# Performance work log

Hardware: AMD Instinct MI355X
Metric: run time of the kernel (lower is better)

Reference implementation:

```python
import jax, jax.numpy as jnp
import numpy as np

DT = 0.005
BETA = 0.9
THR = 0.5
TAU_MIN = 0.02
TAU_STEP = 0.03
TAU_R = 0.002
SLOPE = 25.0  # snntorch fast_sigmoid default surrogate slope

@jax.custom_vjp
def spike_fn(x):
    return (x > 0).astype(x.dtype)

def _spike_fwd(x):
    return spike_fn(x), x

def _spike_bwd(x, g):
    return (g / (SLOPE * jnp.abs(x) + 1.0) ** 2,)

spike_fn.defvjp(_spike_fwd, _spike_bwd)

def setup_inputs() -> dict:
    key = jax.random.key(0)
    ks = jax.random.split(key, 8)
    T, NIN, H, NOUT, P = 1000, 4, 4096, 2, 16
    inv_sqrt_h = 1.0 / np.sqrt(H).astype(np.float32)
    return {
        "x": jax.random.normal(ks[0], (T, NIN + 2, 1), jnp.float32),
        "noise": jax.random.normal(ks[1], (T, H, 1), jnp.float32),
        "Win": jax.random.normal(ks[2], (H, NIN + 2), jnp.float32),
        "Wout": jax.random.normal(ks[3], (NOUT, H), jnp.float32) * inv_sqrt_h,
        "pin": jax.random.normal(ks[4], (H, P), jnp.float32) * inv_sqrt_h,
        "pout": jax.random.normal(ks[5], (H, P), jnp.float32) * inv_sqrt_h,
        "l": jax.random.normal(ks[6], (P,), jnp.float32) * inv_sqrt_h,
        "sigmoid_tau_d": jax.random.normal(ks[7], (H, 1), jnp.float32),
    }

def reference(x, noise, Win, Wout, pin, pout, l, sigmoid_tau_d):
    H = Win.shape[0]
    tau_d = jax.nn.sigmoid(sigmoid_tau_d) * TAU_STEP + TAU_MIN   # [H,1]
    Wr = (l * pin) @ pout.T                                      # [H,H] low-rank recurrent matrix
    decay_r = jnp.exp(jnp.asarray(-DT / TAU_R, x.dtype))         # scalar
    decay_d = jnp.exp(-DT / tau_d)                               # [H,1]
    s_gain = DT / (tau_d * TAU_R)                                # [H,1]

    def step(carry, inp):
        mem, r, s = carry
        xi, ni = inp
        I = Win @ xi + Wr @ r + ni / 10.0                        # [H,1]
        # snntorch Leaky, reset_mechanism='subtract': reset from incoming mem (detached)
        reset = jax.lax.stop_gradient(spike_fn(mem - THR))
        mem = BETA * mem + I - reset * THR
        spk = spike_fn(mem - THR)
        s = s * decay_r + s_gain * spk
        r = decay_d * r + DT * s
        return (mem, r, s), r

    z = jnp.zeros((H, 1), x.dtype)
    _, R = jax.lax.scan(step, (z, z, z), (x, noise))             # R: [T,H,1]
    y = jnp.einsum('oh,thj->toj', Wout, R)                       # [T,O,1]
    return y
```

## Files before the change

kernel.cpp:

```cpp
#include <hip/hip_runtime.h>
#include <math.h>

#define KB       4
#define NBOOT    32
#define NTHREADS 256
#define NW       4
#define HID      4096
#define HB       (HID / KB)
#define NPT      4
#define TT       1000
#define PP       16
#define SLOTW    32

#define BETA 0.9f
#define THRV 0.5f
#define DTV  0.005f

template<int CTRL>
__device__ __forceinline__ float dppx(float v) {
    return __int_as_float(__builtin_amdgcn_update_dpp(
        0, __float_as_int(v), CTRL, 0xF, 0xF, true));
}

__device__ __forceinline__ unsigned long long AL(const unsigned long long* p) {
    return __hip_atomic_load(p, __ATOMIC_RELAXED, __HIP_MEMORY_SCOPE_AGENT);
}
__device__ __forceinline__ void AS(unsigned long long* p, unsigned long long v) {
    __hip_atomic_store(p, v, __ATOMIC_RELAXED, __HIP_MEMORY_SCOPE_AGENT);
}
__device__ __forceinline__ void st64_sc0(unsigned long long* p, unsigned long long v) {
    asm volatile("global_store_dwordx2 %0, %1, off sc0" :: "v"(p), "v"(v) : "memory");
}
__device__ __forceinline__ void rmw3_sc0(unsigned long long* p0,
                                         unsigned long long* p1,
                                         unsigned long long* p2,
                                         unsigned long long& v0,
                                         unsigned long long& v1,
                                         unsigned long long& v2) {
    unsigned long long z = 0;
    asm volatile("global_atomic_add_x2 %0, %3, %6, off sc0\n\t"
                 "global_atomic_add_x2 %1, %4, %6, off sc0\n\t"
                 "global_atomic_add_x2 %2, %5, %6, off sc0\n\t"
                 "s_waitcnt vmcnt(0)"
                 : "=&v"(v0), "=&v"(v1), "=&v"(v2)
                 : "v"(p0), "v"(p1), "v"(p2), "v"(z)
                 : "memory");
}

__global__ void zero_kernel(unsigned* boot) {
    int i = threadIdx.x;
    if (i < NBOOT) boot[i] = 0u;
}

__global__ __launch_bounds__(NTHREADS, 1)
void snn_kernel(const float* __restrict__ x,
                const float* __restrict__ noise,
                const float* __restrict__ Win,
                const float* __restrict__ Wout,
                const float* __restrict__ pin,
                const float* __restrict__ pout,
                const float* __restrict__ lvec,
                const float* __restrict__ stdv,
                float* __restrict__ out,
                unsigned long long* __restrict__ slotsL2,
                unsigned long long* __restrict__ slotsAG,
                unsigned* __restrict__ boot)
{
    const int tid  = threadIdx.x;
    const int wave = tid >> 6;
    const int lane = tid & 63;

    unsigned xcc;
    asm volatile("s_getreg_b32 %0, hwreg(HW_REG_XCC_ID)" : "=s"(xcc));
    if (tid == 0)
        __hip_atomic_store(&boot[blockIdx.x], 0x80000000u | (xcc & 0xffu),
                           __ATOMIC_RELAXED, __HIP_MEMORY_SCOPE_AGENT);
    unsigned e = 0;
    if (lane < NBOOT) {
        int sp = 0;
        do {
            e = __hip_atomic_load(&boot[lane], __ATOMIC_RELAXED,
                                  __HIP_MEMORY_SCOPE_AGENT);
        } while (!(e & 0x80000000u) && ++sp < (1 << 22));
    }
    unsigned long long m = 0; int found = -1;
    #pragma unroll 1
    for (int c = 0; c < 8; ++c) {
        unsigned long long bm = __ballot(lane < NBOOT && (e & 0xffu) == (unsigned)c);
        if (found < 0 && __popcll(bm) >= KB) { m = bm; found = c; }
    }
    if (found < 0) m = 0xFull;
    const int below = __popcll(m & ((1ull << blockIdx.x) - 1ull));
    const bool chosen = ((m >> blockIdx.x) & 1ull) && (below < KB);
    if (!chosen) return;
    const int b = below;

    const int h0 = b * HB + tid * NPT;

    const bool lb0 = (lane & 1) != 0;
    const bool lb1 = (lane & 2) != 0;
    const bool lb2 = (lane & 4) != 0;
    const bool lb3 = (lane & 8) != 0;

    const int rbA = (b == 0) ? 1 : 0;
    const int rbB = (b <= 1) ? 2 : 1;
    const int rbC = (b <= 2) ? 3 : 2;

    __shared__ float part[NW][20];
    __shared__ float ubuf[NW][16];

    float lv[PP];
    #pragma unroll
    for (int p = 0; p < PP; p += 4) {
        float4 t4 = *(const float4*)&lvec[p];
        lv[p] = t4.x; lv[p+1] = t4.y; lv[p+2] = t4.z; lv[p+3] = t4.w;
    }
    float pl[NPT][PP], po[NPT][PP];
    #pragma unroll
    for (int j = 0; j < NPT; ++j) {
        #pragma unroll
        for (int p = 0; p < PP; p += 4) {
            float4 a = *(const float4*)&pin[(h0+j)*PP + p];
            pl[j][p]   = a.x*lv[p];   pl[j][p+1] = a.y*lv[p+1];
            pl[j][p+2] = a.z*lv[p+2]; pl[j][p+3] = a.w*lv[p+3];
            float4 e4 = *(const float4*)&pout[(h0+j)*PP + p];
            po[j][p]   = e4.x; po[j][p+1] = e4.y;
            po[j][p+2] = e4.z; po[j][p+3] = e4.w;
        }
    }
    float win[NPT][6];
    #pragma unroll
    for (int j = 0; j < NPT; ++j) {
        const float2* wr = (const float2*)&Win[(h0+j)*6];
        float2 wA = wr[0], wB = wr[1], wC = wr[2];
        win[j][0]=wA.x; win[j][1]=wA.y; win[j][2]=wB.x;
        win[j][3]=wB.y; win[j][4]=wC.x; win[j][5]=wC.y;
    }
    float4 woa = *(const float4*)&Wout[h0];
    float4 wob = *(const float4*)&Wout[HID + h0];

    float4 sd4 = *(const float4*)&stdv[h0];
    float dd[NPT], sg[NPT];
    {
        float sdv[4] = { sd4.x, sd4.y, sd4.z, sd4.w };
        #pragma unroll
        for (int j = 0; j < NPT; ++j) {
            float sig = 1.f / (1.f + expf(-sdv[j]));
            float tau = sig * 0.03f + 0.02f;
            dd[j] = expf(-DTV / tau);
            sg[j] = DTV / (tau * 0.002f);
        }
    }
    const float DECAY_R = expf(-2.5f);

    float mem[NPT], rr[NPT], ss[NPT], pre[NPT];
    #pragma unroll
    for (int j = 0; j < NPT; ++j) { mem[j] = 0.f; rr[j] = 0.f; ss[j] = 0.f; }

    const float2* x2 = (const float2*)x;
    float4 nz = *(const float4*)&noise[h0];
    float2 xa = x2[0], xb = x2[1], xc = x2[2];

    float uu[16];
    #pragma unroll
    for (int p = 0; p < 16; ++p) uu[p] = 0.f;

    int use_sc0 = 1;

    for (int t = 0; t <= TT; ++t) {
        float4 nz_n = nz; float2 xa_n = xa, xb_n = xb, xc_n = xc;
        if (t < TT - 1) {
            const int tn = t + 1;
            nz_n = *(const float4*)&noise[tn * HID + h0];
            xa_n = x2[tn*3]; xb_n = x2[tn*3+1]; xc_n = x2[tn*3+2];
        }

        float bs = 0.f;
        const int par = t & 1;
        if (t > 0) {
            float pa[18];
            #pragma unroll
            for (int p = 0; p < PP; ++p)
                pa[p] = (po[0][p]*rr[0] + po[1][p]*rr[1])
                      + (po[2][p]*rr[2] + po[3][p]*rr[3]);
            pa[16] = (woa.x*rr[0] + woa.y*rr[1]) + (woa.z*rr[2] + woa.w*rr[3]);
            pa[17] = (wob.x*rr[0] + wob.y*rr[1]) + (wob.z*rr[2] + wob.w*rr[3]);

            float a1[8], yv;
            #pragma unroll
            for (int k = 0; k < 8; ++k) {
                float keep = lb0 ? pa[2*k+1] : pa[2*k];
                float send = lb0 ? pa[2*k]   : pa[2*k+1];
                a1[k] = keep + dppx<0xB1>(send);
            }
            {
                float keep = lb0 ? pa[17] : pa[16];
                float send = lb0 ? pa[16] : pa[17];
                yv = keep + dppx<0xB1>(send);
            }
            float a2[4];
            #pragma unroll
            for (int k = 0; k < 4; ++k) {
                float keep = lb1 ? a1[2*k+1] : a1[2*k];
                float send = lb1 ? a1[2*k]   : a1[2*k+1];
                a2[k] = keep + dppx<0x4E>(send);
            }
            yv += dppx<0x4E>(yv);
            float a3[2];
            #pragma unroll
            for (int k = 0; k < 2; ++k) {
                float keep = lb2 ? a2[2*k+1] : a2[2*k];
                float send = lb2 ? a2[2*k]   : a2[2*k+1];
                a3[k] = keep + __shfl_xor(send, 4, 64);
            }
            yv += __shfl_xor(yv, 4, 64);
            float uv;
            {
                float keep = lb3 ? a3[1] : a3[0];
                float send = lb3 ? a3[0] : a3[1];
                uv = keep + dppx<0x128>(send);
            }
            yv += dppx<0x128>(yv);
            uv += __shfl_xor(uv, 16, 64);
            uv += __shfl_xor(uv, 32, 64);
            yv += __shfl_xor(yv, 16, 64);
            yv += __shfl_xor(yv, 32, 64);

            if (lane < 18) part[wave][lane] = (lane < 16) ? uv : yv;
            __syncthreads();

            if (lane < 18) {
                bs = (part[0][lane] + part[1][lane])
                   + (part[2][lane] + part[3][lane]);
            }

            if (wave == 0 && lane < 18) {
                union { float f; unsigned u; } cv; cv.f = bs;
                unsigned long long pk = ((unsigned long long)(unsigned)t << 32)
                                      | (unsigned long long)cv.u;
                const size_t si = (size_t)(par*KB + b)*SLOTW + lane;
                st64_sc0(&slotsL2[si], pk);
                AS(&slotsAG[si], pk);
            }
        }

        if (t < TT) {
            float nzv[4] = { nz.x, nz.y, nz.z, nz.w };
            #pragma unroll
            for (int j = 0; j < NPT; ++j) {
                float xw = win[j][0]*xa.x + win[j][1]*xa.y
                         + win[j][2]*xb.x + win[j][3]*xb.y
                         + win[j][4]*xc.x + win[j][5]*xc.y;
                float rst = (mem[j] - THRV > 0.f) ? THRV : 0.f;
                pre[j] = BETA*mem[j] + xw + nzv[j] / 10.0f - rst;
            }
        }

        if (t > 0 && (t < TT || b == 0)) {
            const size_t sb = (size_t)par * KB;
            float f0 = 0.f, f1 = 0.f, f2 = 0.f;
            unsigned long long va = 0, vb = 0, vc = 0;
            if (use_sc0) {
                int got = 1;
                if (lane < 18) {
                    unsigned long long* pa_ = &slotsL2[(sb + rbA)*SLOTW + lane];
                    unsigned long long* pb_ = &slotsL2[(sb + rbB)*SLOTW + lane];
                    unsigned long long* pc_ = &slotsL2[(sb + rbC)*SLOTW + lane];
                    const int K = (t == 1) ? 1024 : 64;
                    int sp = 0, ok;
                    do {
                        rmw3_sc0(pa_, pb_, pc_, va, vb, vc);
                        ok = ((unsigned)(va >> 32) == (unsigned)t)
                           & ((unsigned)(vb >> 32) == (unsigned)t)
                           & ((unsigned)(vc >> 32) == (unsigned)t);
                    } while (!ok && ++sp < K);
                    got = ok;
                }
                if (!__all(got)) use_sc0 = 0;
            }
            if (!use_sc0) {
                if (lane < 18) {
                    const unsigned long long* pa_ = &slotsAG[(sb + rbA)*SLOTW + lane];
                    const unsigned long long* pb_ = &slotsAG[(sb + rbB)*SLOTW + lane];
                    const unsigned long long* pc_ = &slotsAG[(sb + rbC)*SLOTW + lane];
                    int sp2 = 0;
                    do {
                        va = AL(pa_); vb = AL(pb_); vc = AL(pc_);
                    } while ((((unsigned)(va >> 32) != (unsigned)t) |
                              ((unsigned)(vb >> 32) != (unsigned)t) |
                              ((unsigned)(vc >> 32) != (unsigned)t)) &&
                             ++sp2 < (1 << 20));
                }
            }
            if (lane < 18) {
                union { unsigned u; float f; } c0, c1, c2;
                c0.u = (unsigned)va; c1.u = (unsigned)vb; c2.u = (unsigned)vc;
                f0 = c0.f; f1 = c1.f; f2 = c2.f;
            }
            float total = (b < 2) ? ((bs + f0) + (f1 + f2))
                                  : ((f0 + f1) + (f2 + bs));
            if (lane < 16) ubuf[wave][lane] = total;
            if (b == 0 && wave == 0 && lane >= 16 && lane < 18)
                out[(t-1)*2 + (lane - 16)] = total;

            float4 u0 = *(const float4*)&ubuf[wave][0];
            float4 u1 = *(const float4*)&ubuf[wave][4];
            float4 u2 = *(const float4*)&ubuf[wave][8];
            float4 u3 = *(const float4*)&ubuf[wave][12];
            uu[0]=u0.x; uu[1]=u0.y; uu[2]=u0.z; uu[3]=u0.w;
            uu[4]=u1.x; uu[5]=u1.y; uu[6]=u1.z; uu[7]=u1.w;
            uu[8]=u2.x; uu[9]=u2.y; uu[10]=u2.z; uu[11]=u2.w;
            uu[12]=u3.x; uu[13]=u3.y; uu[14]=u3.z; uu[15]=u3.w;
        }

        if (t < TT) {
            #pragma unroll
            for (int j = 0; j < NPT; ++j) {
                float ra = pl[j][0]*uu[0];
                float rb2_ = pl[j][8]*uu[8];
                #pragma unroll
                for (int p = 1; p < 8; ++p) {
                    ra   += pl[j][p]*uu[p];
                    rb2_ += pl[j][p+8]*uu[p+8];
                }
                float rec = ra + rb2_;
                mem[j] = pre[j] + rec;
                float spk = (mem[j] - THRV > 0.f) ? 1.f : 0.f;
                ss[j] = ss[j]*DECAY_R + sg[j]*spk;
                rr[j] = dd[j]*rr[j] + DTV*ss[j];
            }
            nz = nz_n; xa = xa_n; xb = xb_n; xc = xc_n;
        }
    }
}

extern "C" void kernel_launch(void* const* d_in, const int* in_sizes, int n_in,
                              void* d_out, int out_size, void* d_ws, size_t ws_size,
                              hipStream_t stream)
{
    const float* x     = (const float*)d_in[0];
    const float* noise = (const float*)d_in[1];
    const float* Win   = (const float*)d_in[2];
    const float* Wout  = (const float*)d_in[3];
    const float* pin   = (const float*)d_in[4];
    const float* pout  = (const float*)d_in[5];
    const float* l     = (const float*)d_in[6];
    const float* stdv  = (const float*)d_in[7];
    float* out = (float*)d_out;
    unsigned long long* slotsL2 = (unsigned long long*)d_ws;
    unsigned long long* slotsAG = (unsigned long long*)((char*)d_ws + 4096);
    unsigned* boot = (unsigned*)((char*)d_ws + 8192);

    hipLaunchKernelGGL(zero_kernel, dim3(1), dim3(64), 0, stream, boot);
    hipLaunchKernelGGL(snn_kernel, dim3(NBOOT), dim3(NTHREADS), 0, stream,
                       x, noise, Win, Wout, pin, pout, l, stdv,
                       out, slotsL2, slotsAG, boot);
}
```

Baseline: 1.629 ms.

## Select co-located blocks by empirical sc0 visibility probing and poll with plain loads

Replaces XCC-ID-based block selection with a timed probe. Each block writes a tagged value with sc0 stores and reads the others' values for a short window, then blocks exchange visibility masks and pick a group of four that mutually see each other. The per-step slot polling switches from zero-add atomics to sc0 loads, with larger spin limits before falling back to agent-scope atomics. The aim is cheaper, more reliable low-latency inter-block exchange over the shared L2, at the cost of a longer startup handshake and a dependence on timing.

New measurement: 1.740 ms. 1.07x slower.

```diff
diff --git a/kernel.cpp b/kernel.cpp
--- a/kernel.cpp
+++ b/kernel.cpp
@@ -31,25 +31,36 @@
 __device__ __forceinline__ void st64_sc0(unsigned long long* p, unsigned long long v) {
     asm volatile("global_store_dwordx2 %0, %1, off sc0" :: "v"(p), "v"(v) : "memory");
 }
-__device__ __forceinline__ void rmw3_sc0(unsigned long long* p0,
-                                         unsigned long long* p1,
-                                         unsigned long long* p2,
-                                         unsigned long long& v0,
-                                         unsigned long long& v1,
-                                         unsigned long long& v2) {
-    unsigned long long z = 0;
-    asm volatile("global_atomic_add_x2 %0, %3, %6, off sc0\n\t"
-                 "global_atomic_add_x2 %1, %4, %6, off sc0\n\t"
-                 "global_atomic_add_x2 %2, %5, %6, off sc0\n\t"
+__device__ __forceinline__ unsigned long long ld64_sc0(const unsigned long long* p) {
+    unsigned long long v;
+    asm volatile("global_load_dwordx2 %0, %1, off sc0\n\ts_waitcnt vmcnt(0)"
+                 : "=v"(v) : "v"(p) : "memory");
+    return v;
+}
+__device__ __forceinline__ void ld64x3_sc0(const unsigned long long* p0,
+                                           const unsigned long long* p1,
+                                           const unsigned long long* p2,
+                                           unsigned long long& v0,
+                                           unsigned long long& v1,
+                                           unsigned long long& v2) {
+    asm volatile("global_load_dwordx2 %0, %3, off sc0\n\t"
+                 "global_load_dwordx2 %1, %4, off sc0\n\t"
+                 "global_load_dwordx2 %2, %5, off sc0\n\t"
                  "s_waitcnt vmcnt(0)"
                  : "=&v"(v0), "=&v"(v1), "=&v"(v2)
-                 : "v"(p0), "v"(p1), "v"(p2), "v"(z)
-                 : "memory");
-}
-
-__global__ void zero_kernel(unsigned* boot) {
+                 : "v"(p0), "v"(p1), "v"(p2) : "memory");
+}
+__device__ __forceinline__ unsigned long long memrealtime() {
+    unsigned long long t;
+    asm volatile("s_memrealtime %0\n\ts_waitcnt lgkmcnt(0)" : "=s"(t));
+    return t;
+}
+
+__global__ void zero_kernel(unsigned long long* probe, unsigned* alive,
+                            unsigned long long* masks) {
     int i = threadIdx.x;
-    if (i < NBOOT) boot[i] = 0u;
+    for (int k = i; k < NBOOT * SLOTW; k += 256) probe[k] = 0ull;
+    if (i < NBOOT) { alive[i] = 0u; masks[i] = 0ull; }
 }
 
 __global__ __launch_bounds__(NTHREADS, 1)
@@ -64,36 +75,68 @@
                 float* __restrict__ out,
                 unsigned long long* __restrict__ slotsL2,
                 unsigned long long* __restrict__ slotsAG,
-                unsigned* __restrict__ boot)
+                unsigned long long* __restrict__ probe,
+                unsigned* __restrict__ alive,
+                unsigned long long* __restrict__ masks)
 {
+    const int bid  = blockIdx.x;
     const int tid  = threadIdx.x;
     const int wave = tid >> 6;
     const int lane = tid & 63;
 
-    unsigned xcc;
-    asm volatile("s_getreg_b32 %0, hwreg(HW_REG_XCC_ID)" : "=s"(xcc));
+    __shared__ float part[NW][20];
+    __shared__ float ubuf[NW][16];
+    __shared__ unsigned mlds[NBOOT];
+
     if (tid == 0)
-        __hip_atomic_store(&boot[blockIdx.x], 0x80000000u | (xcc & 0xffu),
-                           __ATOMIC_RELAXED, __HIP_MEMORY_SCOPE_AGENT);
-    unsigned e = 0;
-    if (lane < NBOOT) {
-        int sp = 0;
+        __hip_atomic_store(&alive[bid], 1u, __ATOMIC_RELAXED, __HIP_MEMORY_SCOPE_AGENT);
+    if (wave == 0) {
+        if (lane < NBOOT) {
+            unsigned a; int sp = 0;
+            do {
+                a = __hip_atomic_load(&alive[lane], __ATOMIC_RELAXED,
+                                      __HIP_MEMORY_SCOPE_AGENT);
+            } while (!a && ++sp < (1 << 22));
+        }
+        const unsigned long long MG = 0xC0DE5EED00000000ull;
+        unsigned seen = 0;
+        unsigned long long t0 = memrealtime();
         do {
-            e = __hip_atomic_load(&boot[lane], __ATOMIC_RELAXED,
-                                  __HIP_MEMORY_SCOPE_AGENT);
-        } while (!(e & 0x80000000u) && ++sp < (1 << 22));
-    }
-    unsigned long long m = 0; int found = -1;
-    #pragma unroll 1
-    for (int c = 0; c < 8; ++c) {
-        unsigned long long bm = __ballot(lane < NBOOT && (e & 0xffu) == (unsigned)c);
-        if (found < 0 && __popcll(bm) >= KB) { m = bm; found = c; }
-    }
-    if (found < 0) m = 0xFull;
-    const int below = __popcll(m & ((1ull << blockIdx.x) - 1ull));
-    const bool chosen = ((m >> blockIdx.x) & 1ull) && (below < KB);
+            if (lane == 0) st64_sc0(&probe[(size_t)bid * SLOTW], MG | (unsigned)bid);
+            unsigned long long v = ld64_sc0(&probe[(size_t)(lane & 31) * SLOTW]);
+            unsigned long long bal =
+                __ballot(v == (MG | (unsigned)(lane & 31)));
+            seen |= (unsigned)(bal | (bal >> 32));
+        } while (memrealtime() - t0 < 500);
+        if (lane == 0)
+            AS(&masks[bid], 0xA11E000000000000ull | (unsigned long long)seen);
+        if (lane < NBOOT) {
+            unsigned long long mv; int sp = 0;
+            do {
+                mv = AL(&masks[lane]);
+            } while (((mv >> 48) != 0xA11Eull) && ++sp < (1 << 22));
+            mlds[lane] = (unsigned)mv;
+        }
+    }
+    __syncthreads();
+
+    int leader = -1; unsigned grp = 0;
+    for (int i = 0; i < NBOOT && leader < 0; ++i) {
+        unsigned mi = mlds[i], mut = 0;
+        for (int j = 0; j < NBOOT; ++j)
+            if (((mi >> j) & 1u) && ((mlds[j] >> i) & 1u)) mut |= (1u << j);
+        if (__popc(mut) >= KB) { leader = i; grp = mut; }
+    }
+    int sc0_ok = 1;
+    if (leader < 0) { grp = 0xFu; sc0_ok = 0; }
+    unsigned g = grp; int ids[4];
+    #pragma unroll
+    for (int k = 0; k < 4; ++k) { ids[k] = __builtin_ctz(g); g &= g - 1; }
+    const bool chosen = (bid == ids[0]) | (bid == ids[1]) |
+                        (bid == ids[2]) | (bid == ids[3]);
     if (!chosen) return;
-    const int b = below;
+    const int b = (bid == ids[0]) ? 0 : (bid == ids[1]) ? 1
+                : (bid == ids[2]) ? 2 : 3;
 
     const int h0 = b * HB + tid * NPT;
 
@@ -105,9 +148,6 @@
     const int rbA = (b == 0) ? 1 : 0;
     const int rbB = (b <= 1) ? 2 : 1;
     const int rbC = (b <= 2) ? 3 : 2;
-
-    __shared__ float part[NW][20];
-    __shared__ float ubuf[NW][16];
 
     float lv[PP];
     #pragma unroll
@@ -165,7 +205,7 @@
     #pragma unroll
     for (int p = 0; p < 16; ++p) uu[p] = 0.f;
 
-    int use_sc0 = 1;
+    int use_sc0 = sc0_ok;
 
     for (int t = 0; t <= TT; ++t) {
         float4 nz_n = nz; float2 xa_n = xa, xb_n = xb, xc_n = xc;
@@ -263,13 +303,13 @@
             if (use_sc0) {
                 int got = 1;
                 if (lane < 18) {
-                    unsigned long long* pa_ = &slotsL2[(sb + rbA)*SLOTW + lane];
-                    unsigned long long* pb_ = &slotsL2[(sb + rbB)*SLOTW + lane];
-                    unsigned long long* pc_ = &slotsL2[(sb + rbC)*SLOTW + lane];
-                    const int K = (t == 1) ? 1024 : 64;
+                    const unsigned long long* pa_ = &slotsL2[(sb + rbA)*SLOTW + lane];
+                    const unsigned long long* pb_ = &slotsL2[(sb + rbB)*SLOTW + lane];
+                    const unsigned long long* pc_ = &slotsL2[(sb + rbC)*SLOTW + lane];
+                    const int K = (t == 1) ? 4096 : 512;
                     int sp = 0, ok;
                     do {
-                        rmw3_sc0(pa_, pb_, pc_, va, vb, vc);
+                        ld64x3_sc0(pa_, pb_, pc_, va, vb, vc);
                         ok = ((unsigned)(va >> 32) == (unsigned)t)
                            & ((unsigned)(vb >> 32) == (unsigned)t)
                            & ((unsigned)(vc >> 32) == (unsigned)t);
@@ -349,10 +389,13 @@
     float* out = (float*)d_out;
     unsigned long long* slotsL2 = (unsigned long long*)d_ws;
     unsigned long long* slotsAG = (unsigned long long*)((char*)d_ws + 4096);
-    unsigned* boot = (unsigned*)((char*)d_ws + 8192);
-
-    hipLaunchKernelGGL(zero_kernel, dim3(1), dim3(64), 0, stream, boot);
+    unsigned long long* probe   = (unsigned long long*)((char*)d_ws + 8192);
+    unsigned*           alive   = (unsigned*)((char*)d_ws + 16384);
+    unsigned long long* masks   = (unsigned long long*)((char*)d_ws + 16640);
+
+    hipLaunchKernelGGL(zero_kernel, dim3(1), dim3(256), 0, stream,
+                       probe, alive, masks);
     hipLaunchKernelGGL(snn_kernel, dim3(NBOOT), dim3(NTHREADS), 0, stream,
                        x, noise, Win, Wout, pin, pout, l, stdv,
-                       out, slotsL2, slotsAG, boot);
-}
+                       out, slotsL2, slotsAG, probe, alive, masks);
+}
```
